# Performance work log

Measured on AMD Instinct MI355X. Metric: run time of the kernel, lower is better.

The kernel has to match this reference:

```python
import jax, jax.numpy as jnp
import numpy as np
from jax.scipy.stats import norm

E = 8          # num experts
R = 16         # LoRA rank
K = 1          # top-k (top-1 gating)
NOISE_EPS = 1e-2


def setup_inputs() -> dict:
    key = jax.random.key(0)
    ks = jax.random.split(key, 6)
    B, T, D = 8, 1024, 1024
    tokens = jax.random.normal(ks[0], (B, T, D), jnp.float32)
    w_gate = jax.random.normal(ks[1], (D, E), jnp.float32) * 0.02
    w_noise = jax.random.normal(ks[2], (D, E), jnp.float32) * 0.02
    lora_a = jax.random.normal(ks[3], (E, R, D), jnp.float32) / np.sqrt(D).astype(np.float32)
    lora_b = jax.random.normal(ks[4], (E, 3 * D, R), jnp.float32) * 0.02
    noise = jax.random.normal(ks[5], (B * T, E), jnp.float32)  # gating noise (randn_like)
    return dict(tokens=tokens, w_gate=w_gate, w_noise=w_noise,
                lora_a=lora_a, lora_b=lora_b, noise=noise)


def reference(tokens, w_gate, w_noise, lora_a, lora_b, noise):
    B, T, D = tokens.shape
    x = tokens.reshape(B * T, D)                       # [N, D]
    N = x.shape[0]

    # --- noisy top-k gating (train mode) ---
    clean_logits = x @ w_gate                          # [N, E]
    noise_stddev = jax.nn.softplus(x @ w_noise) + NOISE_EPS
    logits = clean_logits + noise * noise_stddev       # noisy logits

    m = min(K + 1, E)
    top_vals, top_idx = jax.lax.top_k(logits, m)       # [N, K+1]
    topk_gates = jax.nn.softmax(top_vals[:, :K], axis=1)
    topk_idx = top_idx[:, :K]

    gates = jnp.zeros((N, E), x.dtype).at[jnp.arange(N)[:, None], topk_idx].set(topk_gates)
    importance = gates.sum(0)                          # [E]

    # --- smooth load estimate (prob each token's noisy logit is in top-k) ---
    thr_in = top_vals[:, K][:, None]                   # (K+1)-th value if expert were in
    thr_out = top_vals[:, K - 1][:, None]              # K-th value if expert were out
    is_in = logits > thr_in
    prob = jnp.where(is_in,
                     norm.cdf((clean_logits - thr_in) / noise_stddev),
                     norm.cdf((clean_logits - thr_out) / noise_stddev))
    load = prob.sum(0)                                 # [E]

    # --- dispatch / per-expert LoRA / gated combine ---
    # SparseDispatcher math is equivalent to gate-weighted sum over experts
    # (gates are zero except at the selected experts).
    h = jnp.einsum('nd,erd->ner', x, lora_a)           # [N, E, R] (cheap: R small)
    gh = gates[:, :, None] * h                         # apply gate before up-proj
    out = jnp.einsum('ner,eor->no', gh, lora_b)        # [N, 3D]

    return out.reshape(B, T, 3 * D), importance, load
```

## Files before the change

kernel.cpp:

```cpp
#include <hip/hip_runtime.h>
#include <math.h>

#define N_TOK 8192
#define DIM   1024
#define NE    8
#define NR    16
#define NO    3072
#define OUT_ELEMS (N_TOK * NO)

__device__ __forceinline__ float softplusf(float z) {
  return z > 0.f ? z + log1pf(expf(-z)) : log1pf(expf(z));
}
__device__ __forceinline__ float ncdf(float z) {
  return 0.5f * erfcf(-z * 0.70710678118654752f);
}

#define FMA4(A, S, W) { (A).x = fmaf((S),(W).x,(A).x); (A).y = fmaf((S),(W).y,(A).y); \
                        (A).z = fmaf((S),(W).z,(A).z); (A).w = fmaf((S),(W).w,(A).w); }
#define Z4 make_float4(0.f,0.f,0.f,0.f)

#define DPP_ADD(V, CTRL) ((V) + __int_as_float(__builtin_amdgcn_update_dpp(0, __float_as_int(V), (CTRL), 0xf, 0xf, true)))
#define QRED4(A) { (A).x = DPP_ADD((A).x, 0xB1); (A).y = DPP_ADD((A).y, 0xB1); \
                   (A).z = DPP_ADD((A).z, 0xB1); (A).w = DPP_ADD((A).w, 0xB1); \
                   (A).x = DPP_ADD((A).x, 0x4E); (A).y = DPP_ADD((A).y, 0x4E); \
                   (A).z = DPP_ADD((A).z, 0x4E); (A).w = DPP_ADD((A).w, 0x4E); }

__global__ __launch_bounds__(256) void kA(const float* __restrict__ x,
    const float* __restrict__ wg, const float* __restrict__ wn,
    const float* __restrict__ nz, int* __restrict__ eid, float* __restrict__ part) {
  __shared__ float pd[4][64][20];
  __shared__ float lgS[16][17];
  int t = threadIdx.x;
  int n0 = blockIdx.x << 4;
  int qd = t >> 2, l2 = t & 3, wid = t >> 6, lane = t & 63;
  const float* wgp = wg + (size_t)(t << 2) * NE;
  const float* wnp = wn + (size_t)(t << 2) * NE;
  float4 g0a = *(const float4*)(wgp + 0),  g0b = *(const float4*)(wgp + 4);
  float4 g1a = *(const float4*)(wgp + 8),  g1b = *(const float4*)(wgp + 12);
  float4 g2a = *(const float4*)(wgp + 16), g2b = *(const float4*)(wgp + 20);
  float4 g3a = *(const float4*)(wgp + 24), g3b = *(const float4*)(wgp + 28);
  float4 q0a = *(const float4*)(wnp + 0),  q0b = *(const float4*)(wnp + 4);
  float4 q1a = *(const float4*)(wnp + 8),  q1b = *(const float4*)(wnp + 12);
  float4 q2a = *(const float4*)(wnp + 16), q2b = *(const float4*)(wnp + 20);
  float4 q3a = *(const float4*)(wnp + 24), q3b = *(const float4*)(wnp + 28);
  const float* xb = x + (size_t)n0 * DIM + (t << 2);

  float4 xc0 = *(const float4*)(xb + 0 * DIM);
  float4 xc1 = *(const float4*)(xb + 1 * DIM);
  float4 xc2 = *(const float4*)(xb + 2 * DIM);
  float4 xc3 = *(const float4*)(xb + 3 * DIM);
  #pragma unroll
  for (int b = 0; b < 4; ++b) {
    float4 xn0, xn1, xn2, xn3;
    if (b < 3) {
      const float* xbn = xb + (size_t)((b + 1) << 2) * DIM;
      xn0 = *(const float4*)(xbn + 0 * DIM);
      xn1 = *(const float4*)(xbn + 1 * DIM);
      xn2 = *(const float4*)(xbn + 2 * DIM);
      xn3 = *(const float4*)(xbn + 3 * DIM);
    }
    #define TOKEN(K, XC) { \
      float4 aA = Z4, aB = Z4, aC = Z4, aD = Z4; \
      FMA4(aA, (XC).x, g0a); FMA4(aB, (XC).x, g0b); FMA4(aC, (XC).x, q0a); FMA4(aD, (XC).x, q0b); \
      FMA4(aA, (XC).y, g1a); FMA4(aB, (XC).y, g1b); FMA4(aC, (XC).y, q1a); FMA4(aD, (XC).y, q1b); \
      FMA4(aA, (XC).z, g2a); FMA4(aB, (XC).z, g2b); FMA4(aC, (XC).z, q2a); FMA4(aD, (XC).z, q2b); \
      FMA4(aA, (XC).w, g3a); FMA4(aB, (XC).w, g3b); FMA4(aC, (XC).w, q3a); FMA4(aD, (XC).w, q3b); \
      QRED4(aA); QRED4(aB); QRED4(aC); QRED4(aD); \
      if (l2 == 0) { \
        *(float4*)&pd[K][qd][0]  = aA; *(float4*)&pd[K][qd][4]  = aB; \
        *(float4*)&pd[K][qd][8]  = aC; *(float4*)&pd[K][qd][12] = aD; } }
    TOKEN(0, xc0) TOKEN(1, xc1) TOKEN(2, xc2) TOKEN(3, xc3)
    #undef TOKEN
    __syncthreads();
    {
      int o = lane >> 2, r2 = lane & 3;
      float s = 0.f;
      #pragma unroll
      for (int j = 0; j < 16; ++j) s += pd[wid][(j << 2) + r2][o];
      s = DPP_ADD(s, 0xB1); s = DPP_ADD(s, 0x4E);
      if (r2 == 0) lgS[(b << 2) + wid][o] = s;
    }
    __syncthreads();
    if (b < 3) { xc0 = xn0; xc1 = xn1; xc2 = xn2; xc3 = xn3; }
  }
  if (t < 16) {
    int n = n0 + t;
    float cl[8], st[8], lg[8];
    #pragma unroll
    for (int e = 0; e < 8; ++e) cl[e] = lgS[t][e];
    #pragma unroll
    for (int e = 0; e < 8; ++e) {
      st[e] = softplusf(lgS[t][8 + e]) + 0.01f;
      lg[e] = fmaf(nz[(size_t)n * NE + e], st[e], cl[e]);
    }
    float m1 = -1e30f, m2 = -1e30f; int idx = 0;
    #pragma unroll
    for (int e = 0; e < 8; ++e) {
      float v = lg[e];
      if (v > m1)      { m2 = m1; m1 = v; idx = e; }
      else if (v > m2) { m2 = v; }
    }
    eid[n] = idx;
    float pr[8], cw[8];
    #pragma unroll
    for (int e = 0; e < 8; ++e) {
      float thr = (lg[e] > m2) ? m2 : m1;
      pr[e] = ncdf((cl[e] - thr) / st[e]);
    }
    #pragma unroll
    for (int e = 0; e < 8; ++e) cw[e] = (float)__popcll(__ballot(idx == e));
    #pragma unroll
    for (int e = 0; e < 8; ++e) {
      #pragma unroll
      for (int off = 1; off <= 8; off <<= 1) pr[e] += __shfl_xor(pr[e], off);
    }
    if (t == 0) {
      #pragma unroll
      for (int e = 0; e < 8; ++e) {
        part[blockIdx.x * 16 + e]     = cw[e];
        part[blockIdx.x * 16 + 8 + e] = pr[e];
      }
    }
  }
}

__global__ __launch_bounds__(256) void kB(const float* __restrict__ part,
    float* __restrict__ outIL, int* __restrict__ counts, int* __restrict__ fill) {
  __shared__ float red[16][16];
  int t = threadIdx.x;
  int s = t & 15, g = t >> 4;
  float sum = 0.f;
  for (int j = 0; j < 32; ++j) sum += part[(g + 16 * j) * 16 + s];
  red[g][s] = sum;
  __syncthreads();
  if (t < 16) {
    float tot = 0.f;
    #pragma unroll
    for (int gg = 0; gg < 16; ++gg) tot += red[gg][t];
    outIL[t] = tot;
    if (t < 8) { counts[t] = (int)(tot + 0.5f); fill[t] = 0; }
  }
}

__global__ __launch_bounds__(256) void kC(const int* __restrict__ eid,
    const int* __restrict__ counts, int* __restrict__ fill, int* __restrict__ bucket) {
  __shared__ int lcnt[8], lbase[8];
  int t = threadIdx.x;
  if (t < 8) lcnt[t] = 0;
  __syncthreads();
  int n = blockIdx.x * 256 + t;
  int e = eid[n];
  int rank = atomicAdd(&lcnt[e], 1);
  __syncthreads();
  if (t < 8) lbase[t] = atomicAdd(&fill[t], lcnt[t]);
  __syncthreads();
  int off = 0;
  #pragma unroll
  for (int i = 0; i < 8; ++i) if (i < e) off += counts[i];
  bucket[off + lbase[e] + rank] = n;
}

__global__ __launch_bounds__(256) void kD(const float* __restrict__ x,
    const float* __restrict__ la, const int* __restrict__ counts,
    const int* __restrict__ bucket, float* __restrict__ h) {
  __shared__ float pd[4][64][20];
  __shared__ float hS[16][17];
  __shared__ int toks[16];
  int tile = blockIdx.x;
  int e = -1, jt = 0, off = 0;
  { int tot = 0, o = 0;
    #pragma unroll
    for (int i = 0; i < 8; ++i) {
      int c = counts[i]; int nt = (c + 15) >> 4;
      if (e < 0 && tile < tot + nt) { e = i; jt = tile - tot; off = o; }
      tot += nt; o += c;
    } }
  if (e < 0) return;
  int cnt = counts[e];
  int p0 = off + (jt << 4);
  int valid = min(16, cnt - (jt << 4));
  int t = threadIdx.x;
  if (t < 16) toks[t] = bucket[p0 + min(t, valid - 1)];
  __syncthreads();
  int qd = t >> 2, l2 = t & 3, wid = t >> 6, lane = t & 63;
  const float* ap = la + (size_t)e * NR * DIM + (t << 2);
  float4 w0  = *(const float4*)(ap + 0  * DIM), w1  = *(const float4*)(ap + 1  * DIM);
  float4 w2  = *(const float4*)(ap + 2  * DIM), w3  = *(const float4*)(ap + 3  * DIM);
  float4 w4  = *(const float4*)(ap + 4  * DIM), w5  = *(const float4*)(ap + 5  * DIM);
  float4 w6  = *(const float4*)(ap + 6  * DIM), w7  = *(const float4*)(ap + 7  * DIM);
  float4 w8  = *(const float4*)(ap + 8  * DIM), w9  = *(const float4*)(ap + 9  * DIM);
  float4 w10 = *(const float4*)(ap + 10 * DIM), w11 = *(const float4*)(ap + 11 * DIM);
  float4 w12 = *(const float4*)(ap + 12 * DIM), w13 = *(const float4*)(ap + 13 * DIM);
  float4 w14 = *(const float4*)(ap + 14 * DIM), w15 = *(const float4*)(ap + 15 * DIM);
  int dof = t << 2;
  float4 xc0 = *(const float4*)(x + (size_t)toks[0] * DIM + dof);
  float4 xc1 = *(const float4*)(x + (size_t)toks[1] * DIM + dof);
  float4 xc2 = *(const float4*)(x + (size_t)toks[2] * DIM + dof);
  float4 xc3 = *(const float4*)(x + (size_t)toks[3] * DIM + dof);
  #pragma unroll
  for (int b = 0; b < 4; ++b) {
    float4 xn0, xn1, xn2, xn3;
    if (b < 3) {
      int tb4 = (b + 1) << 2;
      xn0 = *(const float4*)(x + (size_t)toks[tb4 + 0] * DIM + dof);
      xn1 = *(const float4*)(x + (size_t)toks[tb4 + 1] * DIM + dof);
      xn2 = *(const float4*)(x + (size_t)toks[tb4 + 2] * DIM + dof);
      xn3 = *(const float4*)(x + (size_t)toks[tb4 + 3] * DIM + dof);
    }
    #define DOTC(ACC, W, XC) ACC = fmaf((XC).x,(W).x, fmaf((XC).y,(W).y, fmaf((XC).z,(W).z, fmaf((XC).w,(W).w,(ACC)))))
    #define TOKEN(K, XC) { \
      float4 aA = Z4, aB = Z4, aC = Z4, aD = Z4; \
      DOTC(aA.x, w0, XC);  DOTC(aA.y, w1, XC);  DOTC(aA.z, w2, XC);  DOTC(aA.w, w3, XC); \
      DOTC(aB.x, w4, XC);  DOTC(aB.y, w5, XC);  DOTC(aB.z, w6, XC);  DOTC(aB.w, w7, XC); \
      DOTC(aC.x, w8, XC);  DOTC(aC.y, w9, XC);  DOTC(aC.z, w10, XC); DOTC(aC.w, w11, XC); \
      DOTC(aD.x, w12, XC); DOTC(aD.y, w13, XC); DOTC(aD.z, w14, XC); DOTC(aD.w, w15, XC); \
      QRED4(aA); QRED4(aB); QRED4(aC); QRED4(aD); \
      if (l2 == 0) { \
        *(float4*)&pd[K][qd][0]  = aA; *(float4*)&pd[K][qd][4]  = aB; \
        *(float4*)&pd[K][qd][8]  = aC; *(float4*)&pd[K][qd][12] = aD; } }
    TOKEN(0, xc0) TOKEN(1, xc1) TOKEN(2, xc2) TOKEN(3, xc3)
    #undef TOKEN
    #undef DOTC
    __syncthreads();
    { int o = lane >> 2, r2 = lane & 3;
      float s = 0.f;
      #pragma unroll
      for (int j = 0; j < 16; ++j) s += pd[wid][(j << 2) + r2][o];
      s = DPP_ADD(s, 0xB1); s = DPP_ADD(s, 0x4E);
      if (r2 == 0) hS[(b << 2) + wid][o] = s;
    }
    __syncthreads();
    if (b < 3) { xc0 = xn0; xc1 = xn1; xc2 = xn2; xc3 = xn3; }
  }
  if (t < 64) {
    int tok = t >> 2, rq = (t & 3) << 2;
    if (tok < valid) {
      float4 v = make_float4(hS[tok][rq + 0], hS[tok][rq + 1], hS[tok][rq + 2], hS[tok][rq + 3]);
      *(float4*)(h + (size_t)(p0 + tok) * NR + rq) = v;
    }
  }
}

__global__ __launch_bounds__(256) void kE(const float* __restrict__ h,
    const float* __restrict__ lb, const int* __restrict__ counts,
    const int* __restrict__ bucket, float* __restrict__ out) {
  __shared__ float bt[16][260];
  __shared__ float ht[16][64];
  __shared__ int toks[64];
  int tile = blockIdx.y;
  int e = -1, jt = 0, off = 0;
  { int tot = 0, o = 0;
    #pragma unroll
    for (int i = 0; i < 8; ++i) {
      int c = counts[i]; int nt = (c + 63) >> 6;
      if (e < 0 && tile < tot + nt) { e = i; jt = tile - tot; off = o; }
      tot += nt; o += c;
    } }
  if (e < 0) return;
  int cnt = counts[e];
  int p0 = off + (jt << 6);
  int valid = min(64, cnt - (jt << 6));
  int o0 = blockIdx.x << 8;
  int t = threadIdx.x;
  if (t < 64) toks[t] = bucket[p0 + min(t, valid - 1)];
  const float* bbase = lb + ((size_t)e * NO + o0) * NR;
  #pragma unroll
  for (int kk = 0; kk < 4; ++kk) {
    int idx = (kk << 8) + t;
    int o = idx >> 2, rq = (idx & 3) << 2;
    float4 v = *(const float4*)(bbase + o * NR + rq);
    bt[rq + 0][o] = v.x; bt[rq + 1][o] = v.y; bt[rq + 2][o] = v.z; bt[rq + 3][o] = v.w;
  }
  { int tok = t >> 2, rq = (t & 3) << 2;
    float4 v = *(const float4*)(h + (size_t)(p0 + min(tok, valid - 1)) * NR + rq);
    ht[rq + 0][tok] = v.x; ht[rq + 1][tok] = v.y; ht[rq + 2][tok] = v.z; ht[rq + 3][tok] = v.w; }
  __syncthreads();
  int og = t & 31, tokg = t >> 5;
  int ob = og << 2, tb = tokg << 3;
  float4 z = Z4;
  float4 aL0=z,aL1=z,aL2=z,aL3=z,aL4=z,aL5=z,aL6=z,aL7=z;
  float4 aH0=z,aH1=z,aH2=z,aH3=z,aH4=z,aH5=z,aH6=z,aH7=z;
  #pragma unroll
  for (int r = 0; r < 16; ++r) {
    float4 blo = *(const float4*)&bt[r][ob];
    float4 bhi = *(const float4*)&bt[r][ob + 128];
    float4 h0  = *(const float4*)&ht[r][tb];
    float4 h1  = *(const float4*)&ht[r][tb + 4];
    FMA4(aL0, h0.x, blo); FMA4(aH0, h0.x, bhi);
    FMA4(aL1, h0.y, blo); FMA4(aH1, h0.y, bhi);
    FMA4(aL2, h0.z, blo); FMA4(aH2, h0.z, bhi);
    FMA4(aL3, h0.w, blo); FMA4(aH3, h0.w, bhi);
    FMA4(aL4, h1.x, blo); FMA4(aH4, h1.x, bhi);
    FMA4(aL5, h1.y, blo); FMA4(aH5, h1.y, bhi);
    FMA4(aL6, h1.z, blo); FMA4(aH6, h1.z, bhi);
    FMA4(aL7, h1.w, blo); FMA4(aH7, h1.w, bhi);
  }
  #define ST(J, AL, AH) { int tt = tb + (J); if (tt < valid) { \
      float* p = out + (size_t)toks[tt] * NO + o0 + ob; \
      *(float4*)p = AL; *(float4*)(p + 128) = AH; } }
  ST(0, aL0, aH0); ST(1, aL1, aH1); ST(2, aL2, aH2); ST(3, aL3, aH3);
  ST(4, aL4, aH4); ST(5, aL5, aH5); ST(6, aL6, aH6); ST(7, aL7, aH7);
  #undef ST
}

extern "C" void kernel_launch(void* const* d_in, const int* in_sizes, int n_in,
                              void* d_out, int out_size, void* d_ws, size_t ws_size,
                              hipStream_t stream) {
  const float* x  = (const float*)d_in[0];
  const float* wg = (const float*)d_in[1];
  const float* wn = (const float*)d_in[2];
  const float* la = (const float*)d_in[3];
  const float* lb = (const float*)d_in[4];
  const float* nz = (const float*)d_in[5];
  float* out = (float*)d_out;

  char* ws = (char*)d_ws;
  float* h        = (float*)(ws);
  int*   eid      = (int*)  (ws + 524288);
  int*   bucket   = (int*)  (ws + 557056);
  float* partials = (float*)(ws + 589824);
  int*   counts   = (int*)  (ws + 622592);
  int*   fill     = (int*)  (ws + 622624);

  kA<<<512, 256, 0, stream>>>(x, wg, wn, nz, eid, partials);
  kB<<<1, 256, 0, stream>>>(partials, out + OUT_ELEMS, counts, fill);
  kC<<<32, 256, 0, stream>>>(eid, counts, fill, bucket);
  kD<<<519, 256, 0, stream>>>(x, la, counts, bucket, h);
  kE<<<dim3(12, 135), 256, 0, stream>>>(h, lb, counts, bucket, out);
}
```

Measured before the change: 77.53 us.

## Halve tokens per block in gating and LoRA-A kernels, fuse reduction into last block

Gating kernel kA and down-projection kernel kD now process 8 tokens per block instead of 16. This doubles the grid size, and all loads are issued up front rather than through a 4-stage software-pipelined loop, with a launch-bounds occupancy hint added. The separate single-block reduction kernel kB is removed: the last kA block, found through an atomic counter, sums the partials and writes importance/load/counts. This saves one launch but adds a memset and a threadfence/atomic per block. Shared memory per block grows from the larger pd array, which may limit occupancy.

```diff
diff --git a/kernel.cpp b/kernel.cpp
--- a/kernel.cpp
+++ b/kernel.cpp
@@ -7,6 +7,8 @@
 #define NR    16
 #define NO    3072
 #define OUT_ELEMS (N_TOK * NO)
+#define NBLK_A 1024
+#define NBLK_D 1031
 
 __device__ __forceinline__ float softplusf(float z) {
   return z > 0.f ? z + log1pf(expf(-z)) : log1pf(expf(z));
@@ -25,13 +27,17 @@
                    (A).x = DPP_ADD((A).x, 0x4E); (A).y = DPP_ADD((A).y, 0x4E); \
                    (A).z = DPP_ADD((A).z, 0x4E); (A).w = DPP_ADD((A).w, 0x4E); }
 
-__global__ __launch_bounds__(256) void kA(const float* __restrict__ x,
+__global__ __launch_bounds__(256, 3) void kA(const float* __restrict__ x,
     const float* __restrict__ wg, const float* __restrict__ wn,
-    const float* __restrict__ nz, int* __restrict__ eid, float* __restrict__ part) {
-  __shared__ float pd[4][64][20];
-  __shared__ float lgS[16][17];
+    const float* __restrict__ nz, int* __restrict__ eid, float* __restrict__ part,
+    float* __restrict__ outIL, int* __restrict__ counts, int* __restrict__ fill,
+    unsigned int* __restrict__ done) {
+  __shared__ float pd[8][64][20];
+  __shared__ float lgS[8][20];
+  __shared__ float red[16][16];
+  __shared__ int lastFlag;
   int t = threadIdx.x;
-  int n0 = blockIdx.x << 4;
+  int n0 = blockIdx.x << 3;
   int qd = t >> 2, l2 = t & 3, wid = t >> 6, lane = t & 63;
   const float* wgp = wg + (size_t)(t << 2) * NE;
   const float* wnp = wn + (size_t)(t << 2) * NE;
@@ -44,54 +50,51 @@
   float4 q2a = *(const float4*)(wnp + 16), q2b = *(const float4*)(wnp + 20);
   float4 q3a = *(const float4*)(wnp + 24), q3b = *(const float4*)(wnp + 28);
   const float* xb = x + (size_t)n0 * DIM + (t << 2);
-
   float4 xc0 = *(const float4*)(xb + 0 * DIM);
   float4 xc1 = *(const float4*)(xb + 1 * DIM);
   float4 xc2 = *(const float4*)(xb + 2 * DIM);
   float4 xc3 = *(const float4*)(xb + 3 * DIM);
-  #pragma unroll
-  for (int b = 0; b < 4; ++b) {
-    float4 xn0, xn1, xn2, xn3;
-    if (b < 3) {
-      const float* xbn = xb + (size_t)((b + 1) << 2) * DIM;
-      xn0 = *(const float4*)(xbn + 0 * DIM);
-      xn1 = *(const float4*)(xbn + 1 * DIM);
-      xn2 = *(const float4*)(xbn + 2 * DIM);
-      xn3 = *(const float4*)(xbn + 3 * DIM);
-    }
-    #define TOKEN(K, XC) { \
-      float4 aA = Z4, aB = Z4, aC = Z4, aD = Z4; \
-      FMA4(aA, (XC).x, g0a); FMA4(aB, (XC).x, g0b); FMA4(aC, (XC).x, q0a); FMA4(aD, (XC).x, q0b); \
-      FMA4(aA, (XC).y, g1a); FMA4(aB, (XC).y, g1b); FMA4(aC, (XC).y, q1a); FMA4(aD, (XC).y, q1b); \
-      FMA4(aA, (XC).z, g2a); FMA4(aB, (XC).z, g2b); FMA4(aC, (XC).z, q2a); FMA4(aD, (XC).z, q2b); \
-      FMA4(aA, (XC).w, g3a); FMA4(aB, (XC).w, g3b); FMA4(aC, (XC).w, q3a); FMA4(aD, (XC).w, q3b); \
-      QRED4(aA); QRED4(aB); QRED4(aC); QRED4(aD); \
-      if (l2 == 0) { \
-        *(float4*)&pd[K][qd][0]  = aA; *(float4*)&pd[K][qd][4]  = aB; \
-        *(float4*)&pd[K][qd][8]  = aC; *(float4*)&pd[K][qd][12] = aD; } }
-    TOKEN(0, xc0) TOKEN(1, xc1) TOKEN(2, xc2) TOKEN(3, xc3)
-    #undef TOKEN
-    __syncthreads();
-    {
-      int o = lane >> 2, r2 = lane & 3;
-      float s = 0.f;
-      #pragma unroll
-      for (int j = 0; j < 16; ++j) s += pd[wid][(j << 2) + r2][o];
-      s = DPP_ADD(s, 0xB1); s = DPP_ADD(s, 0x4E);
-      if (r2 == 0) lgS[(b << 2) + wid][o] = s;
-    }
-    __syncthreads();
-    if (b < 3) { xc0 = xn0; xc1 = xn1; xc2 = xn2; xc3 = xn3; }
-  }
-  if (t < 16) {
+  float4 xc4 = *(const float4*)(xb + 4 * DIM);
+  float4 xc5 = *(const float4*)(xb + 5 * DIM);
+  float4 xc6 = *(const float4*)(xb + 6 * DIM);
+  float4 xc7 = *(const float4*)(xb + 7 * DIM);
+  #define TOKEN(K, XC) { \
+    float4 aA = Z4, aB = Z4, aC = Z4, aD = Z4; \
+    FMA4(aA, (XC).x, g0a); FMA4(aB, (XC).x, g0b); FMA4(aC, (XC).x, q0a); FMA4(aD, (XC).x, q0b); \
+    FMA4(aA, (XC).y, g1a); FMA4(aB, (XC).y, g1b); FMA4(aC, (XC).y, q1a); FMA4(aD, (XC).y, q1b); \
+    FMA4(aA, (XC).z, g2a); FMA4(aB, (XC).z, g2b); FMA4(aC, (XC).z, q2a); FMA4(aD, (XC).z, q2b); \
+    FMA4(aA, (XC).w, g3a); FMA4(aB, (XC).w, g3b); FMA4(aC, (XC).w, q3a); FMA4(aD, (XC).w, q3b); \
+    QRED4(aA); QRED4(aB); QRED4(aC); QRED4(aD); \
+    if (l2 == 0) { \
+      *(float4*)&pd[K][qd][0]  = aA; *(float4*)&pd[K][qd][4]  = aB; \
+      *(float4*)&pd[K][qd][8]  = aC; *(float4*)&pd[K][qd][12] = aD; } }
+  TOKEN(0, xc0) TOKEN(1, xc1) TOKEN(2, xc2) TOKEN(3, xc3)
+  TOKEN(4, xc4) TOKEN(5, xc5) TOKEN(6, xc6) TOKEN(7, xc7)
+  #undef TOKEN
+  __syncthreads();
+  #pragma unroll
+  for (int rnd = 0; rnd < 2; ++rnd) {
+    int tok = (rnd << 2) + wid;
+    int o = lane >> 2, r2 = lane & 3;
+    float s = 0.f;
+    #pragma unroll
+    for (int j = 0; j < 16; ++j) s += pd[tok][(j << 2) + r2][o];
+    s = DPP_ADD(s, 0xB1); s = DPP_ADD(s, 0x4E);
+    if (r2 == 0) lgS[tok][o] = s;
+  }
+  __syncthreads();
+  if (t < 8) {
     int n = n0 + t;
     float cl[8], st[8], lg[8];
+    float4 nzv0 = *(const float4*)(nz + (size_t)n * NE);
+    float4 nzv1 = *(const float4*)(nz + (size_t)n * NE + 4);
+    float nzv[8] = {nzv0.x, nzv0.y, nzv0.z, nzv0.w, nzv1.x, nzv1.y, nzv1.z, nzv1.w};
     #pragma unroll
     for (int e = 0; e < 8; ++e) cl[e] = lgS[t][e];
     #pragma unroll
     for (int e = 0; e < 8; ++e) {
       st[e] = softplusf(lgS[t][8 + e]) + 0.01f;
-      lg[e] = fmaf(nz[(size_t)n * NE + e], st[e], cl[e]);
+      lg[e] = fmaf(nzv[e], st[e], cl[e]);
     }
     float m1 = -1e30f, m2 = -1e30f; int idx = 0;
     #pragma unroll
@@ -112,7 +115,7 @@
     #pragma unroll
     for (int e = 0; e < 8; ++e) {
       #pragma unroll
-      for (int off = 1; off <= 8; off <<= 1) pr[e] += __shfl_xor(pr[e], off);
+      for (int off = 1; off <= 4; off <<= 1) pr[e] += __shfl_xor(pr[e], off);
     }
     if (t == 0) {
       #pragma unroll
@@ -122,23 +125,27 @@
       }
     }
   }
-}
-
-__global__ __launch_bounds__(256) void kB(const float* __restrict__ part,
-    float* __restrict__ outIL, int* __restrict__ counts, int* __restrict__ fill) {
-  __shared__ float red[16][16];
-  int t = threadIdx.x;
-  int s = t & 15, g = t >> 4;
-  float sum = 0.f;
-  for (int j = 0; j < 32; ++j) sum += part[(g + 16 * j) * 16 + s];
-  red[g][s] = sum;
-  __syncthreads();
-  if (t < 16) {
-    float tot = 0.f;
-    #pragma unroll
-    for (int gg = 0; gg < 16; ++gg) tot += red[gg][t];
-    outIL[t] = tot;
-    if (t < 8) { counts[t] = (int)(tot + 0.5f); fill[t] = 0; }
+  __syncthreads();
+  if (t == 0) {
+    __threadfence();
+    unsigned int old = atomicAdd(done, 1u);
+    lastFlag = (old == NBLK_A - 1) ? 1 : 0;
+  }
+  __syncthreads();
+  if (lastFlag) {
+    __threadfence();
+    int s = t & 15, g = t >> 4;
+    float sum = 0.f;
+    for (int j = 0; j < 64; ++j) sum += part[(g + 16 * j) * 16 + s];
+    red[g][s] = sum;
+    __syncthreads();
+    if (t < 16) {
+      float tot = 0.f;
+      #pragma unroll
+      for (int gg = 0; gg < 16; ++gg) tot += red[gg][t];
+      outIL[t] = tot;
+      if (t < 8) { counts[t] = (int)(tot + 0.5f); fill[t] = 0; }
+    }
   }
 }
 
@@ -160,28 +167,27 @@
   bucket[off + lbase[e] + rank] = n;
 }
 
-__global__ __launch_bounds__(256) void kD(const float* __restrict__ x,
+__global__ __launch_bounds__(256, 3) void kD(const float* __restrict__ x,
     const float* __restrict__ la, const int* __restrict__ counts,
     const int* __restrict__ bucket, float* __restrict__ h) {
-  __shared__ float pd[4][64][20];
-  __shared__ float hS[16][17];
-  __shared__ int toks[16];
+  __shared__ float pd[8][64][20];
+  __shared__ float hS[8][20];
+  __shared__ int toks[8];
   int tile = blockIdx.x;
   int e = -1, jt = 0, off = 0;
   { int tot = 0, o = 0;
     #pragma unroll
     for (int i = 0; i < 8; ++i) {
-      int c = counts[i]; int nt = (c + 15) >> 4;
+      int c = counts[i]; int nt = (c + 7) >> 3;
       if (e < 0 && tile < tot + nt) { e = i; jt = tile - tot; off = o; }
       tot += nt; o += c;
     } }
   if (e < 0) return;
   int cnt = counts[e];
-  int p0 = off + (jt << 4);
-  int valid = min(16, cnt - (jt << 4));
+  int p0 = off + (jt << 3);
+  int valid = min(8, cnt - (jt << 3));
   int t = threadIdx.x;
-  if (t < 16) toks[t] = bucket[p0 + min(t, valid - 1)];
-  __syncthreads();
+  if (t < 8) toks[t] = bucket[p0 + min(t, valid - 1)];
   int qd = t >> 2, l2 = t & 3, wid = t >> 6, lane = t & 63;
   const float* ap = la + (size_t)e * NR * DIM + (t << 2);
   float4 w0  = *(const float4*)(ap + 0  * DIM), w1  = *(const float4*)(ap + 1  * DIM);
@@ -192,47 +198,44 @@
   float4 w10 = *(const float4*)(ap + 10 * DIM), w11 = *(const float4*)(ap + 11 * DIM);
   float4 w12 = *(const float4*)(ap + 12 * DIM), w13 = *(const float4*)(ap + 13 * DIM);
   float4 w14 = *(const float4*)(ap + 14 * DIM), w15 = *(const float4*)(ap + 15 * DIM);
+  __syncthreads();
   int dof = t << 2;
   float4 xc0 = *(const float4*)(x + (size_t)toks[0] * DIM + dof);
   float4 xc1 = *(const float4*)(x + (size_t)toks[1] * DIM + dof);
   float4 xc2 = *(const float4*)(x + (size_t)toks[2] * DIM + dof);
   float4 xc3 = *(const float4*)(x + (size_t)toks[3] * DIM + dof);
-  #pragma unroll
-  for (int b = 0; b < 4; ++b) {
-    float4 xn0, xn1, xn2, xn3;
-    if (b < 3) {
-      int tb4 = (b + 1) << 2;
-      xn0 = *(const float4*)(x + (size_t)toks[tb4 + 0] * DIM + dof);
-      xn1 = *(const float4*)(x + (size_t)toks[tb4 + 1] * DIM + dof);
-      xn2 = *(const float4*)(x + (size_t)toks[tb4 + 2] * DIM + dof);
-      xn3 = *(const float4*)(x + (size_t)toks[tb4 + 3] * DIM + dof);
-    }
-    #define DOTC(ACC, W, XC) ACC = fmaf((XC).x,(W).x, fmaf((XC).y,(W).y, fmaf((XC).z,(W).z, fmaf((XC).w,(W).w,(ACC)))))
-    #define TOKEN(K, XC) { \
-      float4 aA = Z4, aB = Z4, aC = Z4, aD = Z4; \
-      DOTC(aA.x, w0, XC);  DOTC(aA.y, w1, XC);  DOTC(aA.z, w2, XC);  DOTC(aA.w, w3, XC); \
-      DOTC(aB.x, w4, XC);  DOTC(aB.y, w5, XC);  DOTC(aB.z, w6, XC);  DOTC(aB.w, w7, XC); \
-      DOTC(aC.x, w8, XC);  DOTC(aC.y, w9, XC);  DOTC(aC.z, w10, XC); DOTC(aC.w, w11, XC); \
-      DOTC(aD.x, w12, XC); DOTC(aD.y, w13, XC); DOTC(aD.z, w14, XC); DOTC(aD.w, w15, XC); \
-      QRED4(aA); QRED4(aB); QRED4(aC); QRED4(aD); \
-      if (l2 == 0) { \
-        *(float4*)&pd[K][qd][0]  = aA; *(float4*)&pd[K][qd][4]  = aB; \
-        *(float4*)&pd[K][qd][8]  = aC; *(float4*)&pd[K][qd][12] = aD; } }
-    TOKEN(0, xc0) TOKEN(1, xc1) TOKEN(2, xc2) TOKEN(3, xc3)
-    #undef TOKEN
-    #undef DOTC
-    __syncthreads();
-    { int o = lane >> 2, r2 = lane & 3;
-      float s = 0.f;
-      #pragma unroll
-      for (int j = 0; j < 16; ++j) s += pd[wid][(j << 2) + r2][o];
-      s = DPP_ADD(s, 0xB1); s = DPP_ADD(s, 0x4E);
-      if (r2 == 0) hS[(b << 2) + wid][o] = s;
-    }
-    __syncthreads();
-    if (b < 3) { xc0 = xn0; xc1 = xn1; xc2 = xn2; xc3 = xn3; }
-  }
-  if (t < 64) {
+  float4 xc4 = *(const float4*)(x + (size_t)toks[4] * DIM + dof);
+  float4 xc5 = *(const float4*)(x + (size_t)toks[5] * DIM + dof);
+  float4 xc6 = *(const float4*)(x + (size_t)toks[6] * DIM + dof);
+  float4 xc7 = *(const float4*)(x + (size_t)toks[7] * DIM + dof);
+  #define DOTC(ACC, W, XC) ACC = fmaf((XC).x,(W).x, fmaf((XC).y,(W).y, fmaf((XC).z,(W).z, fmaf((XC).w,(W).w,(ACC)))))
+  #define TOKEN(K, XC) { \
+    float4 aA = Z4, aB = Z4, aC = Z4, aD = Z4; \
+    DOTC(aA.x, w0, XC);  DOTC(aA.y, w1, XC);  DOTC(aA.z, w2, XC);  DOTC(aA.w, w3, XC); \
+    DOTC(aB.x, w4, XC);  DOTC(aB.y, w5, XC);  DOTC(aB.z, w6, XC);  DOTC(aB.w, w7, XC); \
+    DOTC(aC.x, w8, XC);  DOTC(aC.y, w9, XC);  DOTC(aC.z, w10, XC); DOTC(aC.w, w11, XC); \
+    DOTC(aD.x, w12, XC); DOTC(aD.y, w13, XC); DOTC(aD.z, w14, XC); DOTC(aD.w, w15, XC); \
+    QRED4(aA); QRED4(aB); QRED4(aC); QRED4(aD); \
+    if (l2 == 0) { \
+      *(float4*)&pd[K][qd][0]  = aA; *(float4*)&pd[K][qd][4]  = aB; \
+      *(float4*)&pd[K][qd][8]  = aC; *(float4*)&pd[K][qd][12] = aD; } }
+  TOKEN(0, xc0) TOKEN(1, xc1) TOKEN(2, xc2) TOKEN(3, xc3)
+  TOKEN(4, xc4) TOKEN(5, xc5) TOKEN(6, xc6) TOKEN(7, xc7)
+  #undef TOKEN
+  #undef DOTC
+  __syncthreads();
+  #pragma unroll
+  for (int rnd = 0; rnd < 2; ++rnd) {
+    int tok = (rnd << 2) + wid;
+    int o = lane >> 2, r2 = lane & 3;
+    float s = 0.f;
+    #pragma unroll
+    for (int j = 0; j < 16; ++j) s += pd[tok][(j << 2) + r2][o];
+    s = DPP_ADD(s, 0xB1); s = DPP_ADD(s, 0x4E);
+    if (r2 == 0) hS[tok][o] = s;
+  }
+  __syncthreads();
+  if (t < 32) {
     int tok = t >> 2, rq = (t & 3) << 2;
     if (tok < valid) {
       float4 v = make_float4(hS[tok][rq + 0], hS[tok][rq + 1], hS[tok][rq + 2], hS[tok][rq + 3]);
@@ -315,16 +318,18 @@
   float* out = (float*)d_out;
 
   char* ws = (char*)d_ws;
-  float* h        = (float*)(ws);
-  int*   eid      = (int*)  (ws + 524288);
-  int*   bucket   = (int*)  (ws + 557056);
-  float* partials = (float*)(ws + 589824);
-  int*   counts   = (int*)  (ws + 622592);
-  int*   fill     = (int*)  (ws + 622624);
-
-  kA<<<512, 256, 0, stream>>>(x, wg, wn, nz, eid, partials);
-  kB<<<1, 256, 0, stream>>>(partials, out + OUT_ELEMS, counts, fill);
+  float*        h        = (float*)(ws);
+  int*          eid      = (int*)  (ws + 524288);
+  int*          bucket   = (int*)  (ws + 557056);
+  float*        partials = (float*)(ws + 589824);
+  int*          counts   = (int*)  (ws + 655360);
+  int*          fill     = (int*)  (ws + 655392);
+  unsigned int* done     = (unsigned int*)(ws + 655424);
+
+  hipMemsetAsync(done, 0, 4, stream);
+  kA<<<NBLK_A, 256, 0, stream>>>(x, wg, wn, nz, eid, partials,
+                                 out + OUT_ELEMS, counts, fill, done);
   kC<<<32, 256, 0, stream>>>(eid, counts, fill, bucket);
-  kD<<<519, 256, 0, stream>>>(x, la, counts, bucket, h);
+  kD<<<NBLK_D, 256, 0, stream>>>(x, la, counts, bucket, h);
   kE<<<dim3(12, 135), 256, 0, stream>>>(h, lb, counts, bucket, out);
 }
```

Result: slower. 98.57 us (+27.1%).

## Stage gate and LoRA-A weights into LDS via global_load_lds, merge reduce/bucket kernels

Applied to the files above, without the earlier changes.

Kernels kA and kD now copy their weight matrices into dynamic shared memory with async global-to-LDS loads before reading them into registers. The token loop processes two tokens per step instead of four. kB's reduction is folded into every kC block, each of which recomputes the global counts redundantly, and the fill counter is reset with a memset, removing one launch. The LDS staging raises shared memory to about 75KB per block, which limits occupancy. It also adds hipFuncSetAttribute calls on every launch and doubles the number of barriers per token.

```diff
diff --git a/kernel.cpp b/kernel.cpp
--- a/kernel.cpp
+++ b/kernel.cpp
@@ -25,73 +25,92 @@
                    (A).x = DPP_ADD((A).x, 0x4E); (A).y = DPP_ADD((A).y, 0x4E); \
                    (A).z = DPP_ADD((A).z, 0x4E); (A).w = DPP_ADD((A).w, 0x4E); }
 
-__global__ __launch_bounds__(256) void kA(const float* __restrict__ x,
+typedef __attribute__((address_space(3))) void LDSV;
+typedef const __attribute__((address_space(1))) void GLBV;
+__device__ __forceinline__ void stage16(const void* g, void* l) {
+  __builtin_amdgcn_global_load_lds((GLBV*)g, (LDSV*)l, 16, 0, 0);
+}
+__device__ __forceinline__ void waitvm0() {
+  asm volatile("s_waitcnt vmcnt(0)" ::: "memory");
+}
+
+#define KA_SMEM (65536 + 8192 + 1088)
+#define KD_SMEM (65536 + 8192 + 1088 + 64)
+
+__global__ __launch_bounds__(256, 2) void kA(const float* __restrict__ x,
     const float* __restrict__ wg, const float* __restrict__ wn,
     const float* __restrict__ nz, int* __restrict__ eid, float* __restrict__ part) {
-  __shared__ float pd[4][64][20];
-  __shared__ float lgS[16][17];
+  extern __shared__ char smem[];
+  float* wgl = (float*)smem;
+  float* wnl = (float*)(smem + 32768);
+  float* pdf = (float*)(smem + 65536);
+  float* lgS = (float*)(smem + 65536 + 8192);
   int t = threadIdx.x;
   int n0 = blockIdx.x << 4;
   int qd = t >> 2, l2 = t & 3, wid = t >> 6, lane = t & 63;
-  const float* wgp = wg + (size_t)(t << 2) * NE;
-  const float* wnp = wn + (size_t)(t << 2) * NE;
-  float4 g0a = *(const float4*)(wgp + 0),  g0b = *(const float4*)(wgp + 4);
-  float4 g1a = *(const float4*)(wgp + 8),  g1b = *(const float4*)(wgp + 12);
-  float4 g2a = *(const float4*)(wgp + 16), g2b = *(const float4*)(wgp + 20);
-  float4 g3a = *(const float4*)(wgp + 24), g3b = *(const float4*)(wgp + 28);
-  float4 q0a = *(const float4*)(wnp + 0),  q0b = *(const float4*)(wnp + 4);
-  float4 q1a = *(const float4*)(wnp + 8),  q1b = *(const float4*)(wnp + 12);
-  float4 q2a = *(const float4*)(wnp + 16), q2b = *(const float4*)(wnp + 20);
-  float4 q3a = *(const float4*)(wnp + 24), q3b = *(const float4*)(wnp + 28);
+  #pragma unroll
+  for (int i = 0; i < 8; ++i) {
+    int s = (i << 8) + t;
+    stage16(wg + ((size_t)s << 2), (char*)wgl + s * 16);
+    stage16(wn + ((size_t)s << 2), (char*)wnl + s * 16);
+  }
+  waitvm0();
+  __syncthreads();
+  float4 g0a = *(const float4*)&wgl[((t << 2) + 0) * NE + 0], g0b = *(const float4*)&wgl[((t << 2) + 0) * NE + 4];
+  float4 g1a = *(const float4*)&wgl[((t << 2) + 1) * NE + 0], g1b = *(const float4*)&wgl[((t << 2) + 1) * NE + 4];
+  float4 g2a = *(const float4*)&wgl[((t << 2) + 2) * NE + 0], g2b = *(const float4*)&wgl[((t << 2) + 2) * NE + 4];
+  float4 g3a = *(const float4*)&wgl[((t << 2) + 3) * NE + 0], g3b = *(const float4*)&wgl[((t << 2) + 3) * NE + 4];
+  float4 q0a = *(const float4*)&wnl[((t << 2) + 0) * NE + 0], q0b = *(const float4*)&wnl[((t << 2) + 0) * NE + 4];
+  float4 q1a = *(const float4*)&wnl[((t << 2) + 1) * NE + 0], q1b = *(const float4*)&wnl[((t << 2) + 1) * NE + 4];
+  float4 q2a = *(const float4*)&wnl[((t << 2) + 2) * NE + 0], q2b = *(const float4*)&wnl[((t << 2) + 2) * NE + 4];
+  float4 q3a = *(const float4*)&wnl[((t << 2) + 3) * NE + 0], q3b = *(const float4*)&wnl[((t << 2) + 3) * NE + 4];
   const float* xb = x + (size_t)n0 * DIM + (t << 2);
-
   float4 xc0 = *(const float4*)(xb + 0 * DIM);
   float4 xc1 = *(const float4*)(xb + 1 * DIM);
-  float4 xc2 = *(const float4*)(xb + 2 * DIM);
-  float4 xc3 = *(const float4*)(xb + 3 * DIM);
-  #pragma unroll
-  for (int b = 0; b < 4; ++b) {
-    float4 xn0, xn1, xn2, xn3;
-    if (b < 3) {
-      const float* xbn = xb + (size_t)((b + 1) << 2) * DIM;
-      xn0 = *(const float4*)(xbn + 0 * DIM);
-      xn1 = *(const float4*)(xbn + 1 * DIM);
-      xn2 = *(const float4*)(xbn + 2 * DIM);
-      xn3 = *(const float4*)(xbn + 3 * DIM);
-    }
-    #define TOKEN(K, XC) { \
-      float4 aA = Z4, aB = Z4, aC = Z4, aD = Z4; \
-      FMA4(aA, (XC).x, g0a); FMA4(aB, (XC).x, g0b); FMA4(aC, (XC).x, q0a); FMA4(aD, (XC).x, q0b); \
-      FMA4(aA, (XC).y, g1a); FMA4(aB, (XC).y, g1b); FMA4(aC, (XC).y, q1a); FMA4(aD, (XC).y, q1b); \
-      FMA4(aA, (XC).z, g2a); FMA4(aB, (XC).z, g2b); FMA4(aC, (XC).z, q2a); FMA4(aD, (XC).z, q2b); \
-      FMA4(aA, (XC).w, g3a); FMA4(aB, (XC).w, g3b); FMA4(aC, (XC).w, q3a); FMA4(aD, (XC).w, q3b); \
-      QRED4(aA); QRED4(aB); QRED4(aC); QRED4(aD); \
-      if (l2 == 0) { \
-        *(float4*)&pd[K][qd][0]  = aA; *(float4*)&pd[K][qd][4]  = aB; \
-        *(float4*)&pd[K][qd][8]  = aC; *(float4*)&pd[K][qd][12] = aD; } }
-    TOKEN(0, xc0) TOKEN(1, xc1) TOKEN(2, xc2) TOKEN(3, xc3)
-    #undef TOKEN
+  #define TOKEN(K, XC) { \
+    float4 aA = Z4, aB = Z4, aC = Z4, aD = Z4; \
+    FMA4(aA, (XC).x, g0a); FMA4(aB, (XC).x, g0b); FMA4(aC, (XC).x, q0a); FMA4(aD, (XC).x, q0b); \
+    FMA4(aA, (XC).y, g1a); FMA4(aB, (XC).y, g1b); FMA4(aC, (XC).y, q1a); FMA4(aD, (XC).y, q1b); \
+    FMA4(aA, (XC).z, g2a); FMA4(aB, (XC).z, g2b); FMA4(aC, (XC).z, q2a); FMA4(aD, (XC).z, q2b); \
+    FMA4(aA, (XC).w, g3a); FMA4(aB, (XC).w, g3b); FMA4(aC, (XC).w, q3a); FMA4(aD, (XC).w, q3b); \
+    QRED4(aA); QRED4(aB); QRED4(aC); QRED4(aD); \
+    if (l2 == 0) { \
+      float* p_ = pdf + ((((K) << 6) + qd) << 4); \
+      *(float4*)(p_ + 0) = aA; *(float4*)(p_ + 4)  = aB; \
+      *(float4*)(p_ + 8) = aC; *(float4*)(p_ + 12) = aD; } }
+  for (int r = 0; r < 8; ++r) {
+    float4 xn0, xn1;
+    if (r < 7) {
+      xn0 = *(const float4*)(xb + (size_t)((r << 1) + 2) * DIM);
+      xn1 = *(const float4*)(xb + (size_t)((r << 1) + 3) * DIM);
+    }
+    TOKEN(0, xc0)
+    TOKEN(1, xc1)
     __syncthreads();
-    {
+    if (wid < 2) {
       int o = lane >> 2, r2 = lane & 3;
-      float s = 0.f;
+      float s2 = 0.f;
       #pragma unroll
-      for (int j = 0; j < 16; ++j) s += pd[wid][(j << 2) + r2][o];
-      s = DPP_ADD(s, 0xB1); s = DPP_ADD(s, 0x4E);
-      if (r2 == 0) lgS[(b << 2) + wid][o] = s;
+      for (int j = 0; j < 16; ++j) s2 += pdf[((wid << 6) + (j << 2) + r2) * 16 + o];
+      s2 = DPP_ADD(s2, 0xB1); s2 = DPP_ADD(s2, 0x4E);
+      if (r2 == 0) lgS[((r << 1) + wid) * 17 + o] = s2;
     }
     __syncthreads();
-    if (b < 3) { xc0 = xn0; xc1 = xn1; xc2 = xn2; xc3 = xn3; }
-  }
+    xc0 = xn0; xc1 = xn1;
+  }
+  #undef TOKEN
   if (t < 16) {
     int n = n0 + t;
     float cl[8], st[8], lg[8];
-    #pragma unroll
-    for (int e = 0; e < 8; ++e) cl[e] = lgS[t][e];
+    float4 nzv0 = *(const float4*)(nz + (size_t)n * NE);
+    float4 nzv1 = *(const float4*)(nz + (size_t)n * NE + 4);
+    float nzv[8] = {nzv0.x, nzv0.y, nzv0.z, nzv0.w, nzv1.x, nzv1.y, nzv1.z, nzv1.w};
+    #pragma unroll
+    for (int e = 0; e < 8; ++e) cl[e] = lgS[t * 17 + e];
     #pragma unroll
     for (int e = 0; e < 8; ++e) {
-      st[e] = softplusf(lgS[t][8 + e]) + 0.01f;
-      lg[e] = fmaf(nz[(size_t)n * NE + e], st[e], cl[e]);
+      st[e] = softplusf(lgS[t * 17 + 8 + e]) + 0.01f;
+      lg[e] = fmaf(nzv[e], st[e], cl[e]);
     }
     float m1 = -1e30f, m2 = -1e30f; int idx = 0;
     #pragma unroll
@@ -124,29 +143,29 @@
   }
 }
 
-__global__ __launch_bounds__(256) void kB(const float* __restrict__ part,
-    float* __restrict__ outIL, int* __restrict__ counts, int* __restrict__ fill) {
+__global__ __launch_bounds__(256) void kC(const float* __restrict__ part,
+    const int* __restrict__ eid, int* __restrict__ fill, int* __restrict__ bucket,
+    float* __restrict__ outIL, int* __restrict__ counts) {
   __shared__ float red[16][16];
+  __shared__ int cnt_s[8], lcnt[8], lbase[8];
   int t = threadIdx.x;
   int s = t & 15, g = t >> 4;
   float sum = 0.f;
+  #pragma unroll
   for (int j = 0; j < 32; ++j) sum += part[(g + 16 * j) * 16 + s];
   red[g][s] = sum;
+  if (t < 8) lcnt[t] = 0;
   __syncthreads();
   if (t < 16) {
     float tot = 0.f;
     #pragma unroll
     for (int gg = 0; gg < 16; ++gg) tot += red[gg][t];
-    outIL[t] = tot;
-    if (t < 8) { counts[t] = (int)(tot + 0.5f); fill[t] = 0; }
-  }
-}
-
-__global__ __launch_bounds__(256) void kC(const int* __restrict__ eid,
-    const int* __restrict__ counts, int* __restrict__ fill, int* __restrict__ bucket) {
-  __shared__ int lcnt[8], lbase[8];
-  int t = threadIdx.x;
-  if (t < 8) lcnt[t] = 0;
+    if (blockIdx.x == 0) outIL[t] = tot;
+    if (t < 8) {
+      cnt_s[t] = (int)(tot + 0.5f);
+      if (blockIdx.x == 0) counts[t] = (int)(tot + 0.5f);
+    }
+  }
   __syncthreads();
   int n = blockIdx.x * 256 + t;
   int e = eid[n];
@@ -156,16 +175,18 @@
   __syncthreads();
   int off = 0;
   #pragma unroll
-  for (int i = 0; i < 8; ++i) if (i < e) off += counts[i];
+  for (int i = 0; i < 8; ++i) if (i < e) off += cnt_s[i];
   bucket[off + lbase[e] + rank] = n;
 }
 
-__global__ __launch_bounds__(256) void kD(const float* __restrict__ x,
+__global__ __launch_bounds__(256, 2) void kD(const float* __restrict__ x,
     const float* __restrict__ la, const int* __restrict__ counts,
     const int* __restrict__ bucket, float* __restrict__ h) {
-  __shared__ float pd[4][64][20];
-  __shared__ float hS[16][17];
-  __shared__ int toks[16];
+  extern __shared__ char smem[];
+  float* lal = (float*)smem;
+  float* pdf = (float*)(smem + 65536);
+  float* hS  = (float*)(smem + 65536 + 8192);
+  int*  toks = (int*)(smem + 65536 + 8192 + 1088);
   int tile = blockIdx.x;
   int e = -1, jt = 0, off = 0;
   { int tot = 0, o = 0;
@@ -181,61 +202,72 @@
   int valid = min(16, cnt - (jt << 4));
   int t = threadIdx.x;
   if (t < 16) toks[t] = bucket[p0 + min(t, valid - 1)];
+  #pragma unroll
+  for (int i = 0; i < 16; ++i) {
+    int s = (i << 8) + t;
+    stage16(la + (size_t)e * (NR * DIM) + ((size_t)s << 2), (char*)lal + s * 16);
+  }
+  waitvm0();
   __syncthreads();
   int qd = t >> 2, l2 = t & 3, wid = t >> 6, lane = t & 63;
-  const float* ap = la + (size_t)e * NR * DIM + (t << 2);
-  float4 w0  = *(const float4*)(ap + 0  * DIM), w1  = *(const float4*)(ap + 1  * DIM);
-  float4 w2  = *(const float4*)(ap + 2  * DIM), w3  = *(const float4*)(ap + 3  * DIM);
-  float4 w4  = *(const float4*)(ap + 4  * DIM), w5  = *(const float4*)(ap + 5  * DIM);
-  float4 w6  = *(const float4*)(ap + 6  * DIM), w7  = *(const float4*)(ap + 7  * DIM);
-  float4 w8  = *(const float4*)(ap + 8  * DIM), w9  = *(const float4*)(ap + 9  * DIM);
-  float4 w10 = *(const float4*)(ap + 10 * DIM), w11 = *(const float4*)(ap + 11 * DIM);
-  float4 w12 = *(const float4*)(ap + 12 * DIM), w13 = *(const float4*)(ap + 13 * DIM);
-  float4 w14 = *(const float4*)(ap + 14 * DIM), w15 = *(const float4*)(ap + 15 * DIM);
+  float4 w0  = *(const float4*)&lal[0  * DIM + (t << 2)];
+  float4 w1  = *(const float4*)&lal[1  * DIM + (t << 2)];
+  float4 w2  = *(const float4*)&lal[2  * DIM + (t << 2)];
+  float4 w3  = *(const float4*)&lal[3  * DIM + (t << 2)];
+  float4 w4  = *(const float4*)&lal[4  * DIM + (t << 2)];
+  float4 w5  = *(const float4*)&lal[5  * DIM + (t << 2)];
+  float4 w6  = *(const float4*)&lal[6  * DIM + (t << 2)];
+  float4 w7  = *(const float4*)&lal[7  * DIM + (t << 2)];
+  float4 w8  = *(const float4*)&lal[8  * DIM + (t << 2)];
+  float4 w9  = *(const float4*)&lal[9  * DIM + (t << 2)];
+  float4 w10 = *(const float4*)&lal[10 * DIM + (t << 2)];
+  float4 w11 = *(const float4*)&lal[11 * DIM + (t << 2)];
+  float4 w12 = *(const float4*)&lal[12 * DIM + (t << 2)];
+  float4 w13 = *(const float4*)&lal[13 * DIM + (t << 2)];
+  float4 w14 = *(const float4*)&lal[14 * DIM + (t << 2)];
+  float4 w15 = *(const float4*)&lal[15 * DIM + (t << 2)];
   int dof = t << 2;
   float4 xc0 = *(const float4*)(x + (size_t)toks[0] * DIM + dof);
   float4 xc1 = *(const float4*)(x + (size_t)toks[1] * DIM + dof);
-  float4 xc2 = *(const float4*)(x + (size_t)toks[2] * DIM + dof);
-  float4 xc3 = *(const float4*)(x + (size_t)toks[3] * DIM + dof);
-  #pragma unroll
-  for (int b = 0; b < 4; ++b) {
-    float4 xn0, xn1, xn2, xn3;
-    if (b < 3) {
-      int tb4 = (b + 1) << 2;
-      xn0 = *(const float4*)(x + (size_t)toks[tb4 + 0] * DIM + dof);
-      xn1 = *(const float4*)(x + (size_t)toks[tb4 + 1] * DIM + dof);
-      xn2 = *(const float4*)(x + (size_t)toks[tb4 + 2] * DIM + dof);
-      xn3 = *(const float4*)(x + (size_t)toks[tb4 + 3] * DIM + dof);
-    }
-    #define DOTC(ACC, W, XC) ACC = fmaf((XC).x,(W).x, fmaf((XC).y,(W).y, fmaf((XC).z,(W).z, fmaf((XC).w,(W).w,(ACC)))))
-    #define TOKEN(K, XC) { \
-      float4 aA = Z4, aB = Z4, aC = Z4, aD = Z4; \
-      DOTC(aA.x, w0, XC);  DOTC(aA.y, w1, XC);  DOTC(aA.z, w2, XC);  DOTC(aA.w, w3, XC); \
-      DOTC(aB.x, w4, XC);  DOTC(aB.y, w5, XC);  DOTC(aB.z, w6, XC);  DOTC(aB.w, w7, XC); \
-      DOTC(aC.x, w8, XC);  DOTC(aC.y, w9, XC);  DOTC(aC.z, w10, XC); DOTC(aC.w, w11, XC); \
-      DOTC(aD.x, w12, XC); DOTC(aD.y, w13, XC); DOTC(aD.z, w14, XC); DOTC(aD.w, w15, XC); \
-      QRED4(aA); QRED4(aB); QRED4(aC); QRED4(aD); \
-      if (l2 == 0) { \
-        *(float4*)&pd[K][qd][0]  = aA; *(float4*)&pd[K][qd][4]  = aB; \
-        *(float4*)&pd[K][qd][8]  = aC; *(float4*)&pd[K][qd][12] = aD; } }
-    TOKEN(0, xc0) TOKEN(1, xc1) TOKEN(2, xc2) TOKEN(3, xc3)
-    #undef TOKEN
-    #undef DOTC
+  #define DOTC(ACC, W, XC) ACC = fmaf((XC).x,(W).x, fmaf((XC).y,(W).y, fmaf((XC).z,(W).z, fmaf((XC).w,(W).w,(ACC)))))
+  #define TOKEN(K, XC) { \
+    float4 aA = Z4, aB = Z4, aC = Z4, aD = Z4; \
+    DOTC(aA.x, w0, XC);  DOTC(aA.y, w1, XC);  DOTC(aA.z, w2, XC);  DOTC(aA.w, w3, XC); \
+    DOTC(aB.x, w4, XC);  DOTC(aB.y, w5, XC);  DOTC(aB.z, w6, XC);  DOTC(aB.w, w7, XC); \
+    DOTC(aC.x, w8, XC);  DOTC(aC.y, w9, XC);  DOTC(aC.z, w10, XC); DOTC(aC.w, w11, XC); \
+    DOTC(aD.x, w12, XC); DOTC(aD.y, w13, XC); DOTC(aD.z, w14, XC); DOTC(aD.w, w15, XC); \
+    QRED4(aA); QRED4(aB); QRED4(aC); QRED4(aD); \
+    if (l2 == 0) { \
+      float* p_ = pdf + ((((K) << 6) + qd) << 4); \
+      *(float4*)(p_ + 0) = aA; *(float4*)(p_ + 4)  = aB; \
+      *(float4*)(p_ + 8) = aC; *(float4*)(p_ + 12) = aD; } }
+  for (int r = 0; r < 8; ++r) {
+    float4 xn0, xn1;
+    if (r < 7) {
+      xn0 = *(const float4*)(x + (size_t)toks[(r << 1) + 2] * DIM + dof);
+      xn1 = *(const float4*)(x + (size_t)toks[(r << 1) + 3] * DIM + dof);
+    }
+    TOKEN(0, xc0)
+    TOKEN(1, xc1)
     __syncthreads();
-    { int o = lane >> 2, r2 = lane & 3;
-      float s = 0.f;
+    if (wid < 2) {
+      int o = lane >> 2, r2 = lane & 3;
+      float s2 = 0.f;
       #pragma unroll
-      for (int j = 0; j < 16; ++j) s += pd[wid][(j << 2) + r2][o];
-      s = DPP_ADD(s, 0xB1); s = DPP_ADD(s, 0x4E);
-      if (r2 == 0) hS[(b << 2) + wid][o] = s;
+      for (int j = 0; j < 16; ++j) s2 += pdf[((wid << 6) + (j << 2) + r2) * 16 + o];
+      s2 = DPP_ADD(s2, 0xB1); s2 = DPP_ADD(s2, 0x4E);
+      if (r2 == 0) hS[((r << 1) + wid) * 17 + o] = s2;
     }
     __syncthreads();
-    if (b < 3) { xc0 = xn0; xc1 = xn1; xc2 = xn2; xc3 = xn3; }
-  }
+    xc0 = xn0; xc1 = xn1;
+  }
+  #undef TOKEN
+  #undef DOTC
   if (t < 64) {
     int tok = t >> 2, rq = (t & 3) << 2;
     if (tok < valid) {
-      float4 v = make_float4(hS[tok][rq + 0], hS[tok][rq + 1], hS[tok][rq + 2], hS[tok][rq + 3]);
+      float4 v = make_float4(hS[tok * 17 + rq + 0], hS[tok * 17 + rq + 1],
+                             hS[tok * 17 + rq + 2], hS[tok * 17 + rq + 3]);
       *(float4*)(h + (size_t)(p0 + tok) * NR + rq) = v;
     }
   }
@@ -322,9 +354,11 @@
   int*   counts   = (int*)  (ws + 622592);
   int*   fill     = (int*)  (ws + 622624);
 
-  kA<<<512, 256, 0, stream>>>(x, wg, wn, nz, eid, partials);
-  kB<<<1, 256, 0, stream>>>(partials, out + OUT_ELEMS, counts, fill);
-  kC<<<32, 256, 0, stream>>>(eid, counts, fill, bucket);
-  kD<<<519, 256, 0, stream>>>(x, la, counts, bucket, h);
+  hipFuncSetAttribute((const void*)kA, hipFuncAttributeMaxDynamicSharedMemorySize, KA_SMEM);
+  hipFuncSetAttribute((const void*)kD, hipFuncAttributeMaxDynamicSharedMemorySize, KD_SMEM);
+  hipMemsetAsync(fill, 0, 32, stream);
+  kA<<<512, 256, KA_SMEM, stream>>>(x, wg, wn, nz, eid, partials);
+  kC<<<32, 256, 0, stream>>>(partials, eid, fill, bucket, out + OUT_ELEMS, counts);
+  kD<<<519, 256, KD_SMEM, stream>>>(x, la, counts, bucket, h);
   kE<<<dim3(12, 135), 256, 0, stream>>>(h, lb, counts, bucket, out);
 }
```

Measured after the change: 83.30 us. 1.07x slower.
